# Optimization experiments

Hardware: AMD Instinct MI355X
Metric: run time of the kernel (lower is better)

## Reference

```python
import jax, jax.numpy as jnp
import numpy as np

T = 2.0          # hardcoded in __init__ (self.T = 2)
EPSILON = 0.1    # sinkhorn_loss default
N_ITERS = 10     # sinkhorn_loss default passed to sinkhorn_normalized
COST_CLIP = 10.0
TINY = 1e-8

B, S, V = 16, 512, 4096


def setup_inputs() -> dict:
    key = jax.random.key(0)
    k1, k2 = jax.random.split(key)
    y_s = jax.random.normal(k1, (B, S, V), dtype=jnp.float32)
    y_t = jax.random.normal(k2, (B, S, V), dtype=jnp.float32)
    return {"y_s": y_s, "y_t": y_t}


def _cdist_l1(x, y):
    # x, y: [S, V] -> [S, S]; row-streamed via lax.map to avoid a [S,S,V] intermediate
    return jax.lax.map(lambda xi: jnp.sum(jnp.abs(xi[None, :] - y), axis=-1), x)


def _sinkhorn_loss(x, y):
    # x, y: [S, V] softmax probabilities for one sample
    Wxy = _cdist_l1(x, y)                                  # [S, S]
    K = jnp.exp(-jnp.minimum(Wxy, COST_CLIP) / EPSILON)
    P = jnp.nan_to_num(K, nan=TINY, posinf=1e6, neginf=-1e6) + TINY
    for _ in range(N_ITERS):
        P = P / jnp.maximum(jnp.sum(P, axis=1, keepdims=True), TINY)
        P = jnp.nan_to_num(P, nan=TINY)
        P = P / jnp.maximum(jnp.sum(P, axis=0, keepdims=True), TINY)
        P = jnp.nan_to_num(P, nan=TINY)
    return jnp.sum(P * Wxy)


def reference(y_s, y_t):
    p_s = jax.nn.softmax(y_s / T, axis=-1)
    p_t = jax.nn.softmax(y_t / T, axis=-1)
    p_s = jnp.nan_to_num(p_s, nan=TINY)
    p_t = jnp.nan_to_num(p_t, nan=TINY)
    per_sample = jax.vmap(_sinkhorn_loss)(p_s, p_t)        # [B]
    # forward accumulates 0.001 * loss_i and divides by the number of valid samples
    return jnp.mean(0.001 * per_sample)
```

## Files before the change

kernel.cpp:

```cpp
#include <hip/hip_runtime.h>

#define B_ 16
#define S_ 512
#define V_ 4096

typedef unsigned int uint;
typedef unsigned short ushort;
typedef unsigned char u8;


__device__ __forceinline__ uint sad8(uint a, uint b, uint c) {
#if __has_builtin(__builtin_amdgcn_sad_u8)
    return __builtin_amdgcn_sad_u8(a, b, c);
#else
    uint s = c;
#pragma unroll
    for (int i = 0; i < 4; ++i) {
        uint x = (a >> (8 * i)) & 0xFFu, y = (b >> (8 * i)) & 0xFFu;
        s += x > y ? x - y : y - x;
    }
    return s;
#endif
}

__device__ __forceinline__ float bflo(uint p) { return __uint_as_float(p << 16); }
__device__ __forceinline__ float bfhi(uint p) { return __uint_as_float(p & 0xFFFF0000u); }

__device__ __forceinline__ ushort f2bf(float f) {
    uint u = __float_as_uint(f);
    u = (u + 0x7FFFu + ((u >> 16) & 1u)) >> 16;
    return (ushort)u;
}

__device__ __forceinline__ float waveMax(float v) {
#pragma unroll
    for (int o = 32; o; o >>= 1) v = fmaxf(v, __shfl_xor(v, o, 64));
    return v;
}
__device__ __forceinline__ float waveSum(float v) {
#pragma unroll
    for (int o = 32; o; o >>= 1) v += __shfl_xor(v, o, 64);
    return v;
}

#define QSCALE 65536.0f
#define QINV   1.52587890625e-5f

__global__ __launch_bounds__(256) void softmax_kernel(
        const float* __restrict__ ys, const float* __restrict__ yt,
        u8* __restrict__ qs, u8* __restrict__ qt) {
    const int row = blockIdx.x;
    const float* in = blockIdx.y ? yt : ys;
    u8* out = blockIdx.y ? qt : qs;
    const float* px = in + (size_t)row * V_;
    u8* po = out + (size_t)row * V_;
    const int tid = threadIdx.x;

    float4 v4[4];
    float m = -3.4e38f;
#pragma unroll
    for (int i = 0; i < 4; ++i) {
        v4[i] = ((const float4*)px)[tid + 256 * i];
        m = fmaxf(m, fmaxf(fmaxf(v4[i].x, v4[i].y), fmaxf(v4[i].z, v4[i].w)));
    }
    __shared__ float redm[4], reds[4];
    float wm = waveMax(m);
    if ((tid & 63) == 0) redm[tid >> 6] = wm;
    __syncthreads();
    const float rm = fmaxf(fmaxf(redm[0], redm[1]), fmaxf(redm[2], redm[3]));

    float e[16];
    float s = 0.f;
#pragma unroll
    for (int i = 0; i < 4; ++i) {
        const float* f = (const float*)&v4[i];
#pragma unroll
        for (int k = 0; k < 4; ++k) {
            float ev = __expf((f[k] - rm) * 0.5f);
            e[i * 4 + k] = ev;
            s += ev;
        }
    }
    float wsm = waveSum(s);
    if ((tid & 63) == 0) reds[tid >> 6] = wsm;
    __syncthreads();
    const float inv = 1.0f / (reds[0] + reds[1] + reds[2] + reds[3]);

#pragma unroll
    for (int i = 0; i < 4; ++i) {
        uint pk = 0;
#pragma unroll
        for (int k = 0; k < 4; ++k) {
            float p = e[i * 4 + k] * inv;
            uint q = (uint)fminf(p * QSCALE + 0.5f, 255.f);
            pk |= q << (8 * k);
        }
        ((uint*)po)[tid + 256 * i] = pk;
    }
}

#define TI 128
#define TJ 128
#define KCB 128
#define LDPB 144

__global__ __launch_bounds__(256) void pairwise_kernel(
        const u8* __restrict__ qs, const u8* __restrict__ qt,
        uint* __restrict__ Acc) {
    const int bz = blockIdx.z;
    const int b = bz >> 2, vq = bz & 3;
    const int tR = blockIdx.y * TI;
    const int tC = blockIdx.x * TJ;
    const u8* xrow = qs + (size_t)b * S_ * V_;
    const u8* yrow = qt + (size_t)b * S_ * V_;
    const int tid = threadIdx.x;
    const int tx = tid & 15, ty = tid >> 4;
    const int kbase = vq * (V_ / 4);

    __shared__ u8 xs[TI * LDPB];
    __shared__ u8 ysm[TJ * LDPB];

    uint acc[8][8];
#pragma unroll
    for (int r = 0; r < 8; ++r)
#pragma unroll
        for (int c = 0; c < 8; ++c) acc[r][c] = 0u;

    for (int k0 = 0; k0 < V_ / 4; k0 += KCB) {
#pragma unroll
        for (int m = tid; m < TI * 8; m += 256) {
            const int r = m >> 3, c = m & 7;
            *(uint4*)&xs[r * LDPB + c * 16] =
                *(const uint4*)&xrow[(size_t)(tR + r) * V_ + kbase + k0 + c * 16];
        }
#pragma unroll
        for (int m = tid; m < TJ * 8; m += 256) {
            const int r = m >> 3, c = m & 7;
            *(uint4*)&ysm[r * LDPB + c * 16] =
                *(const uint4*)&yrow[(size_t)(tC + r) * V_ + kbase + k0 + c * 16];
        }
        __syncthreads();

#pragma unroll 2
        for (int kk = 0; kk < KCB; kk += 16) {
            uint4 Af[8], Bf[8];
#pragma unroll
            for (int r = 0; r < 8; ++r)
                Af[r] = *(const uint4*)&xs[(ty + 16 * r) * LDPB + kk];
#pragma unroll
            for (int c = 0; c < 8; ++c)
                Bf[c] = *(const uint4*)&ysm[(tx + 16 * c) * LDPB + kk];
#pragma unroll
            for (int r = 0; r < 8; ++r)
#pragma unroll
                for (int c = 0; c < 8; ++c) {
                    uint t = sad8(Af[r].x, Bf[c].x, acc[r][c]);
                    t = sad8(Af[r].y, Bf[c].y, t);
                    t = sad8(Af[r].z, Bf[c].z, t);
                    acc[r][c] = sad8(Af[r].w, Bf[c].w, t);
                }
        }
        __syncthreads();
    }

#pragma unroll
    for (int r = 0; r < 8; ++r) {
        const int i = tR + ty + 16 * r;
        const size_t base = ((size_t)b * S_ + i) * S_;
#pragma unroll
        for (int c = 0; c < 8; ++c) {
            const int j = tC + tx + 16 * c;
            atomicAdd(&Acc[base + j], acc[r][c]);
        }
    }
}

__global__ __launch_bounds__(256) void pairwise_epi(
        const uint* __restrict__ Acc, ushort* __restrict__ Wb,
        ushort* __restrict__ Kb) {
    const size_t g = (size_t)blockIdx.x * 256 + threadIdx.x;
    uint4 a = ((const uint4*)Acc)[g];
    union { uint2 u; ushort h[4]; } pw, pk;
    uint av[4] = {a.x, a.y, a.z, a.w};
#pragma unroll
    for (int t = 0; t < 4; ++t) {
        float w = fminf((float)av[t] * QINV, 10.f);
        pw.h[t] = f2bf(w);
        pk.h[t] = f2bf(__expf(-10.f * w) + 1e-8f);
    }
    ((uint2*)Wb)[g] = pw.u;
    ((uint2*)Kb)[g] = pk.u;
}

__global__ __launch_bounds__(1024) void sink_block(
        const ushort* __restrict__ Kb, const ushort* __restrict__ Wb,
        float* __restrict__ out) {
    const int b = blockIdx.x;
    const int tid = threadIdx.x, lane = tid & 63, wv = tid >> 6;

    __shared__ float vls[S_];
    __shared__ float uls[S_];
    __shared__ float cw[16][S_];
    __shared__ float redw[16];

    if (tid < S_) { vls[tid] = 1.f; uls[tid] = 1.f; }
    __syncthreads();

    const ushort* Kbase = Kb + (size_t)b * S_ * S_ + (size_t)lane * 8;

    for (int k = 0; k < 10; ++k) {
        const float4 va  = *(const float4*)&vls[lane * 8];
        const float4 vb4 = *(const float4*)&vls[lane * 8 + 4];
        float cs0 = 0.f, cs1 = 0.f, cs2 = 0.f, cs3 = 0.f;
        float cs4 = 0.f, cs5 = 0.f, cs6 = 0.f, cs7 = 0.f;
#pragma unroll 4
        for (int r = 0; r < 32; ++r) {
            const int i = wv * 32 + r;
            const uint4 kq = *(const uint4*)&Kbase[(size_t)i * S_];
            const float k0 = bflo(kq.x), k1 = bfhi(kq.x);
            const float k2 = bflo(kq.y), k3 = bfhi(kq.y);
            const float k4 = bflo(kq.z), k5 = bfhi(kq.z);
            const float k6 = bflo(kq.w), k7 = bfhi(kq.w);
            float acc = 0.f;
            acc = fmaf(k0, va.x, acc);  acc = fmaf(k1, va.y, acc);
            acc = fmaf(k2, va.z, acc);  acc = fmaf(k3, va.w, acc);
            acc = fmaf(k4, vb4.x, acc); acc = fmaf(k5, vb4.y, acc);
            acc = fmaf(k6, vb4.z, acc); acc = fmaf(k7, vb4.w, acc);
            const float rs = waveSum(acc);
            const float up = uls[i];
            const float un = up / fmaxf(up * rs, 1e-8f);
            if (lane == 0) uls[i] = un;
            cs0 = fmaf(un, k0, cs0); cs1 = fmaf(un, k1, cs1);
            cs2 = fmaf(un, k2, cs2); cs3 = fmaf(un, k3, cs3);
            cs4 = fmaf(un, k4, cs4); cs5 = fmaf(un, k5, cs5);
            cs6 = fmaf(un, k6, cs6); cs7 = fmaf(un, k7, cs7);
        }
        *(float4*)&cw[wv][lane * 8]     = make_float4(cs0, cs1, cs2, cs3);
        *(float4*)&cw[wv][lane * 8 + 4] = make_float4(cs4, cs5, cs6, cs7);
        __syncthreads();
        if (tid < S_) {
            float s = 0.f;
#pragma unroll
            for (int t = 0; t < 16; ++t) s += cw[t][tid];
            const float vp = vls[tid];
            vls[tid] = vp / fmaxf(vp * s, 1e-8f);
        }
        __syncthreads();
    }

    const float4 va  = *(const float4*)&vls[lane * 8];
    const float4 vb4 = *(const float4*)&vls[lane * 8 + 4];
    const ushort* Wbase = Wb + (size_t)b * S_ * S_ + (size_t)lane * 8;
    float accl = 0.f;
#pragma unroll 2
    for (int r = 0; r < 32; ++r) {
        const int i = wv * 32 + r;
        const uint4 kq = *(const uint4*)&Kbase[(size_t)i * S_];
        const uint4 wq = *(const uint4*)&Wbase[(size_t)i * S_];
        float rp = 0.f;
        rp = fmaf(bflo(kq.x) * va.x,  bflo(wq.x), rp);
        rp = fmaf(bfhi(kq.x) * va.y,  bfhi(wq.x), rp);
        rp = fmaf(bflo(kq.y) * va.z,  bflo(wq.y), rp);
        rp = fmaf(bfhi(kq.y) * va.w,  bfhi(wq.y), rp);
        rp = fmaf(bflo(kq.z) * vb4.x, bflo(wq.z), rp);
        rp = fmaf(bfhi(kq.z) * vb4.y, bfhi(wq.z), rp);
        rp = fmaf(bflo(kq.w) * vb4.z, bflo(wq.w), rp);
        rp = fmaf(bfhi(kq.w) * vb4.w, bfhi(wq.w), rp);
        accl = fmaf(uls[i], rp, accl);
    }
    accl = waveSum(accl);
    if (lane == 0) redw[wv] = accl;
    __syncthreads();
    if (tid == 0) {
        float s = 0.f;
#pragma unroll
        for (int t = 0; t < 16; ++t) s += redw[t];
        atomicAdd(out, s * (0.001f / 16.f));
    }
}

extern "C" void kernel_launch(void* const* d_in, const int* in_sizes, int n_in,
                              void* d_out, int out_size, void* d_ws, size_t ws_size,
                              hipStream_t stream) {
    const float* ys = (const float*)d_in[0];
    const float* yt = (const float*)d_in[1];
    float* out = (float*)d_out;

    char* w = (char*)d_ws;
    u8* qs = (u8*)w;
    u8* qt = qs + (size_t)B_ * S_ * V_;
    uint* Acc = (uint*)(qt + (size_t)B_ * S_ * V_);
    ushort* Wb = (ushort*)qs;
    ushort* Kb = Wb + (size_t)B_ * S_ * S_;

    (void)hipMemsetAsync(Acc, 0, (size_t)B_ * S_ * S_ * 4, stream);
    (void)hipMemsetAsync(out, 0, sizeof(float), stream);

    softmax_kernel<<<dim3(8192, 2), 256, 0, stream>>>(ys, yt, qs, qt);
    pairwise_kernel<<<dim3(4, 4, 64), 256, 0, stream>>>(qs, qt, Acc);
    pairwise_epi<<<4096, 256, 0, stream>>>(Acc, Wb, Kb);
    sink_block<<<16, 1024, 0, stream>>>(Kb, Wb, out);
}
```

Before: 624.6 us.

## Prefetch pairwise tiles into registers and regroup Sinkhorn lanes into row quads

The pairwise SAD kernel now works on half-size K chunks and prefetches the next chunk from global memory into registers while the current one is being computed, so the load loop no longer sits in series with the compute. Launch bounds are raised to allow more resident blocks. The Sinkhorn kernel changes its lane mapping: each wave now handles four rows at once, with 16 lanes per row and 32 columns per lane. This replaces the full 64-lane reduction per row with a 16-lane shuffle reduction, and the column sums are reduced across row quads with shuffles into a padded shared buffer. The cost is higher register pressure (32-element vr and cs arrays), which could cut occupancy or cause spills.

```diff
diff --git a/kernel.cpp b/kernel.cpp
--- a/kernel.cpp
+++ b/kernel.cpp
@@ -101,45 +101,56 @@
 
 #define TI 128
 #define TJ 128
-#define KCB 128
-#define LDPB 144
-
-__global__ __launch_bounds__(256) void pairwise_kernel(
+#define KCB 64
+#define LDPB 80
+
+__global__ __launch_bounds__(256, 4) void pairwise_kernel(
         const u8* __restrict__ qs, const u8* __restrict__ qt,
         uint* __restrict__ Acc) {
     const int bz = blockIdx.z;
     const int b = bz >> 2, vq = bz & 3;
     const int tR = blockIdx.y * TI;
     const int tC = blockIdx.x * TJ;
-    const u8* xrow = qs + (size_t)b * S_ * V_;
-    const u8* yrow = qt + (size_t)b * S_ * V_;
+    const u8* xrow = qs + (size_t)b * S_ * V_ + vq * (V_ / 4);
+    const u8* yrow = qt + (size_t)b * S_ * V_ + vq * (V_ / 4);
     const int tid = threadIdx.x;
     const int tx = tid & 15, ty = tid >> 4;
-    const int kbase = vq * (V_ / 4);
 
     __shared__ u8 xs[TI * LDPB];
     __shared__ u8 ysm[TJ * LDPB];
 
+    const int r0 = tid >> 2, c0 = tid & 3;
+    const u8* xA = xrow + (size_t)(tR + r0) * V_ + c0 * 16;
+    const u8* xB = xA + (size_t)64 * V_;
+    const u8* yA = yrow + (size_t)(tC + r0) * V_ + c0 * 16;
+    const u8* yB = yA + (size_t)64 * V_;
+    const int lw0 = r0 * LDPB + c0 * 16;
+    const int lw1 = (r0 + 64) * LDPB + c0 * 16;
+
     uint acc[8][8];
 #pragma unroll
     for (int r = 0; r < 8; ++r)
 #pragma unroll
         for (int c = 0; c < 8; ++c) acc[r][c] = 0u;
 
+    {
+        uint4 a = *(const uint4*)xA, bq = *(const uint4*)xB;
+        uint4 cq = *(const uint4*)yA, d = *(const uint4*)yB;
+        *(uint4*)&xs[lw0] = a;  *(uint4*)&xs[lw1] = bq;
+        *(uint4*)&ysm[lw0] = cq; *(uint4*)&ysm[lw1] = d;
+    }
+    __syncthreads();
+
     for (int k0 = 0; k0 < V_ / 4; k0 += KCB) {
-#pragma unroll
-        for (int m = tid; m < TI * 8; m += 256) {
-            const int r = m >> 3, c = m & 7;
-            *(uint4*)&xs[r * LDPB + c * 16] =
-                *(const uint4*)&xrow[(size_t)(tR + r) * V_ + kbase + k0 + c * 16];
-        }
-#pragma unroll
-        for (int m = tid; m < TJ * 8; m += 256) {
-            const int r = m >> 3, c = m & 7;
-            *(uint4*)&ysm[r * LDPB + c * 16] =
-                *(const uint4*)&yrow[(size_t)(tC + r) * V_ + kbase + k0 + c * 16];
-        }
-        __syncthreads();
+        const int kn = k0 + KCB;
+        uint4 nxA, nxB, nyA, nyB;
+        const bool more = kn < V_ / 4;
+        if (more) {
+            nxA = *(const uint4*)(xA + kn);
+            nxB = *(const uint4*)(xB + kn);
+            nyA = *(const uint4*)(yA + kn);
+            nyB = *(const uint4*)(yB + kn);
+        }
 
 #pragma unroll 2
         for (int kk = 0; kk < KCB; kk += 16) {
@@ -161,6 +172,11 @@
                 }
         }
         __syncthreads();
+        if (more) {
+            *(uint4*)&xs[lw0] = nxA;  *(uint4*)&xs[lw1] = nxB;
+            *(uint4*)&ysm[lw0] = nyA; *(uint4*)&ysm[lw1] = nyB;
+            __syncthreads();
+        }
     }
 
 #pragma unroll
@@ -192,81 +208,139 @@
     ((uint2*)Kb)[g] = pk.u;
 }
 
-__global__ __launch_bounds__(1024) void sink_block(
+#define VPAD 36
+
+__global__ __launch_bounds__(1024, 4) void sink_block(
         const ushort* __restrict__ Kb, const ushort* __restrict__ Wb,
         float* __restrict__ out) {
     const int b = blockIdx.x;
     const int tid = threadIdx.x, lane = tid & 63, wv = tid >> 6;
-
-    __shared__ float vls[S_];
+    const int ch = lane & 15, rq = lane >> 4;
+
+    __shared__ float vp[16 * VPAD];
     __shared__ float uls[S_];
-    __shared__ float cw[16][S_];
+    __shared__ float cwp[16][16 * VPAD];
     __shared__ float redw[16];
 
-    if (tid < S_) { vls[tid] = 1.f; uls[tid] = 1.f; }
-    __syncthreads();
-
-    const ushort* Kbase = Kb + (size_t)b * S_ * S_ + (size_t)lane * 8;
-
-    for (int k = 0; k < 10; ++k) {
-        const float4 va  = *(const float4*)&vls[lane * 8];
-        const float4 vb4 = *(const float4*)&vls[lane * 8 + 4];
-        float cs0 = 0.f, cs1 = 0.f, cs2 = 0.f, cs3 = 0.f;
-        float cs4 = 0.f, cs5 = 0.f, cs6 = 0.f, cs7 = 0.f;
-#pragma unroll 4
-        for (int r = 0; r < 32; ++r) {
-            const int i = wv * 32 + r;
-            const uint4 kq = *(const uint4*)&Kbase[(size_t)i * S_];
-            const float k0 = bflo(kq.x), k1 = bfhi(kq.x);
-            const float k2 = bflo(kq.y), k3 = bfhi(kq.y);
-            const float k4 = bflo(kq.z), k5 = bfhi(kq.z);
-            const float k6 = bflo(kq.w), k7 = bfhi(kq.w);
-            float acc = 0.f;
-            acc = fmaf(k0, va.x, acc);  acc = fmaf(k1, va.y, acc);
-            acc = fmaf(k2, va.z, acc);  acc = fmaf(k3, va.w, acc);
-            acc = fmaf(k4, vb4.x, acc); acc = fmaf(k5, vb4.y, acc);
-            acc = fmaf(k6, vb4.z, acc); acc = fmaf(k7, vb4.w, acc);
-            const float rs = waveSum(acc);
+    for (int m = tid; m < 16 * VPAD; m += 1024) vp[m] = 1.f;
+    if (tid < S_) uls[tid] = 1.f;
+    __syncthreads();
+
+    const ushort* Kl = Kb + (size_t)b * S_ * S_;
+    const int chB = ch * 32;
+    const int vpB = ch * VPAD;
+
+    for (int it = 0; it < 10; ++it) {
+        float vr[32];
+#pragma unroll
+        for (int q = 0; q < 8; ++q)
+            *(float4*)&vr[q * 4] = *(const float4*)&vp[vpB + q * 4];
+
+        float cs[32];
+#pragma unroll
+        for (int k = 0; k < 32; ++k) cs[k] = 0.f;
+
+#pragma unroll 2
+        for (int g = 0; g < 8; ++g) {
+            const int i = wv * 32 + g * 4 + rq;
+            const ushort* kp = Kl + (size_t)i * S_ + chB;
+            uint4 kq[4];
+            kq[0] = *(const uint4*)kp;
+            kq[1] = *(const uint4*)(kp + 8);
+            kq[2] = *(const uint4*)(kp + 16);
+            kq[3] = *(const uint4*)(kp + 24);
+            float dot = 0.f;
+#pragma unroll
+            for (int q = 0; q < 4; ++q) {
+                const uint x0 = kq[q].x, x1 = kq[q].y, x2 = kq[q].z, x3 = kq[q].w;
+                dot = fmaf(bflo(x0), vr[q * 8 + 0], dot);
+                dot = fmaf(bfhi(x0), vr[q * 8 + 1], dot);
+                dot = fmaf(bflo(x1), vr[q * 8 + 2], dot);
+                dot = fmaf(bfhi(x1), vr[q * 8 + 3], dot);
+                dot = fmaf(bflo(x2), vr[q * 8 + 4], dot);
+                dot = fmaf(bfhi(x2), vr[q * 8 + 5], dot);
+                dot = fmaf(bflo(x3), vr[q * 8 + 6], dot);
+                dot = fmaf(bfhi(x3), vr[q * 8 + 7], dot);
+            }
+            dot += __shfl_xor(dot, 1, 64);
+            dot += __shfl_xor(dot, 2, 64);
+            dot += __shfl_xor(dot, 4, 64);
+            dot += __shfl_xor(dot, 8, 64);
             const float up = uls[i];
-            const float un = up / fmaxf(up * rs, 1e-8f);
-            if (lane == 0) uls[i] = un;
-            cs0 = fmaf(un, k0, cs0); cs1 = fmaf(un, k1, cs1);
-            cs2 = fmaf(un, k2, cs2); cs3 = fmaf(un, k3, cs3);
-            cs4 = fmaf(un, k4, cs4); cs5 = fmaf(un, k5, cs5);
-            cs6 = fmaf(un, k6, cs6); cs7 = fmaf(un, k7, cs7);
-        }
-        *(float4*)&cw[wv][lane * 8]     = make_float4(cs0, cs1, cs2, cs3);
-        *(float4*)&cw[wv][lane * 8 + 4] = make_float4(cs4, cs5, cs6, cs7);
+            const float un = up / fmaxf(up * dot, 1e-8f);
+            if (ch == 0) uls[i] = un;
+#pragma unroll
+            for (int q = 0; q < 4; ++q) {
+                const uint x0 = kq[q].x, x1 = kq[q].y, x2 = kq[q].z, x3 = kq[q].w;
+                cs[q * 8 + 0] = fmaf(un, bflo(x0), cs[q * 8 + 0]);
+                cs[q * 8 + 1] = fmaf(un, bfhi(x0), cs[q * 8 + 1]);
+                cs[q * 8 + 2] = fmaf(un, bflo(x1), cs[q * 8 + 2]);
+                cs[q * 8 + 3] = fmaf(un, bfhi(x1), cs[q * 8 + 3]);
+                cs[q * 8 + 4] = fmaf(un, bflo(x2), cs[q * 8 + 4]);
+                cs[q * 8 + 5] = fmaf(un, bfhi(x2), cs[q * 8 + 5]);
+                cs[q * 8 + 6] = fmaf(un, bflo(x3), cs[q * 8 + 6]);
+                cs[q * 8 + 7] = fmaf(un, bfhi(x3), cs[q * 8 + 7]);
+            }
+        }
+#pragma unroll
+        for (int k = 0; k < 32; ++k) cs[k] += __shfl_xor(cs[k], 16, 64);
+#pragma unroll
+        for (int k = 0; k < 32; ++k) cs[k] += __shfl_xor(cs[k], 32, 64);
+        if (rq == 0) {
+#pragma unroll
+            for (int q = 0; q < 8; ++q)
+                *(float4*)&cwp[wv][vpB + q * 4] =
+                    make_float4(cs[q * 4 + 0], cs[q * 4 + 1],
+                                cs[q * 4 + 2], cs[q * 4 + 3]);
+        }
         __syncthreads();
         if (tid < S_) {
+            const int a = (tid >> 5) * VPAD + (tid & 31);
             float s = 0.f;
 #pragma unroll
-            for (int t = 0; t < 16; ++t) s += cw[t][tid];
-            const float vp = vls[tid];
-            vls[tid] = vp / fmaxf(vp * s, 1e-8f);
+            for (int t = 0; t < 16; ++t) s += cwp[t][a];
+            const float vv = vp[a];
+            vp[a] = vv / fmaxf(vv * s, 1e-8f);
         }
         __syncthreads();
     }
 
-    const float4 va  = *(const float4*)&vls[lane * 8];
-    const float4 vb4 = *(const float4*)&vls[lane * 8 + 4];
-    const ushort* Wbase = Wb + (size_t)b * S_ * S_ + (size_t)lane * 8;
+    float vr[32];
+#pragma unroll
+    for (int q = 0; q < 8; ++q)
+        *(float4*)&vr[q * 4] = *(const float4*)&vp[vpB + q * 4];
+    const ushort* Wl = Wb + (size_t)b * S_ * S_;
     float accl = 0.f;
 #pragma unroll 2
-    for (int r = 0; r < 32; ++r) {
-        const int i = wv * 32 + r;
-        const uint4 kq = *(const uint4*)&Kbase[(size_t)i * S_];
-        const uint4 wq = *(const uint4*)&Wbase[(size_t)i * S_];
+    for (int g = 0; g < 8; ++g) {
+        const int i = wv * 32 + g * 4 + rq;
+        const ushort* kp = Kl + (size_t)i * S_ + chB;
+        const ushort* wp = Wl + (size_t)i * S_ + chB;
+        uint4 kq[4], wq[4];
+#pragma unroll
+        for (int q = 0; q < 4; ++q) {
+            kq[q] = *(const uint4*)(kp + q * 8);
+            wq[q] = *(const uint4*)(wp + q * 8);
+        }
         float rp = 0.f;
-        rp = fmaf(bflo(kq.x) * va.x,  bflo(wq.x), rp);
-        rp = fmaf(bfhi(kq.x) * va.y,  bfhi(wq.x), rp);
-        rp = fmaf(bflo(kq.y) * va.z,  bflo(wq.y), rp);
-        rp = fmaf(bfhi(kq.y) * va.w,  bfhi(wq.y), rp);
-        rp = fmaf(bflo(kq.z) * vb4.x, bflo(wq.z), rp);
-        rp = fmaf(bfhi(kq.z) * vb4.y, bfhi(wq.z), rp);
-        rp = fmaf(bflo(kq.w) * vb4.z, bflo(wq.w), rp);
-        rp = fmaf(bfhi(kq.w) * vb4.w, bfhi(wq.w), rp);
-        accl = fmaf(uls[i], rp, accl);
+#pragma unroll
+        for (int q = 0; q < 4; ++q) {
+            const uint k0 = kq[q].x, k1 = kq[q].y, k2 = kq[q].z, k3 = kq[q].w;
+            const uint w0 = wq[q].x, w1 = wq[q].y, w2 = wq[q].z, w3 = wq[q].w;
+            rp = fmaf(bflo(k0) * vr[q * 8 + 0], bflo(w0), rp);
+            rp = fmaf(bfhi(k0) * vr[q * 8 + 1], bfhi(w0), rp);
+            rp = fmaf(bflo(k1) * vr[q * 8 + 2], bflo(w1), rp);
+            rp = fmaf(bfhi(k1) * vr[q * 8 + 3], bfhi(w1), rp);
+            rp = fmaf(bflo(k2) * vr[q * 8 + 4], bflo(w2), rp);
+            rp = fmaf(bfhi(k2) * vr[q * 8 + 5], bfhi(w2), rp);
+            rp = fmaf(bflo(k3) * vr[q * 8 + 6], bflo(w3), rp);
+            rp = fmaf(bfhi(k3) * vr[q * 8 + 7], bfhi(w3), rp);
+        }
+        rp += __shfl_xor(rp, 1, 64);
+        rp += __shfl_xor(rp, 2, 64);
+        rp += __shfl_xor(rp, 4, 64);
+        rp += __shfl_xor(rp, 8, 64);
+        if (ch == 0) accl = fmaf(uls[i], rp, accl);
     }
     accl = waveSum(accl);
     if (lane == 0) redw[wv] = accl;
```

New measurement: 720.4 us. 1.15x slower.
